# Optimization experiments

Hardware: AMD Instinct MI355X
Metric: run time of the kernel (lower is better)

Reference implementation:

```python
import jax, jax.numpy as jnp
import numpy as np

N, E, D_IN, HD, H = 50000, 800000, 768, 64, 4
HC = HD * H


def _gat(x, src, dst, etypes, lin_w, att_src, att_dst, edge_emb, lin_edge_w, att_edge,
         bias, res_w, res_b, ln_g, ln_b):
    # Faithful PyG GATConv (edge_dim, concat=True, add_self_loops=True with
    # fill_value='mean', negative_slope=0.2) + residual + LayerNorm. Eval mode: no dropout.
    n = x.shape[0]
    h, c = att_src.shape
    xs = (x @ lin_w).reshape(n, h, c)                      # [N,H,C]
    a_src = jnp.einsum('nhc,hc->nh', xs, att_src)          # [N,H]
    a_dst = jnp.einsum('nhc,hc->nh', xs, att_dst)
    eattr = edge_emb[etypes]                               # [E,ed]
    ones = jnp.ones((etypes.shape[0],), x.dtype)
    cnt = jax.ops.segment_sum(ones, dst, num_segments=n)
    # self-loop edge_attr = mean of incoming edge attrs per node (fill_value='mean')
    loop_attr = jax.ops.segment_sum(eattr, dst, num_segments=n) / jnp.maximum(cnt, 1.0)[:, None]
    loop = jnp.arange(n, dtype=src.dtype)
    src_a = jnp.concatenate([src, loop])
    dst_a = jnp.concatenate([dst, loop])
    e_all = jnp.concatenate([eattr, loop_attr], 0)
    a_edge = jnp.einsum('ehc,hc->eh', (e_all @ lin_edge_w).reshape(-1, h, c), att_edge)
    alpha = jax.nn.leaky_relu(a_src[src_a] + a_dst[dst_a] + a_edge, 0.2)   # [Ea,H]
    # edge softmax over incoming edges of each destination node
    amax = jax.ops.segment_max(alpha, dst_a, num_segments=n)
    ea = jnp.exp(alpha - amax[dst_a])
    denom = jax.ops.segment_sum(ea, dst_a, num_segments=n)
    w = ea / (denom[dst_a] + 1e-16)
    out = jax.ops.segment_sum(xs[src_a] * w[:, :, None], dst_a, num_segments=n)
    out = out.reshape(n, h * c) + bias + (x @ res_w + res_b)
    mu = out.mean(-1, keepdims=True)
    var = jnp.mean((out - mu) ** 2, -1, keepdims=True)
    return (out - mu) * jax.lax.rsqrt(var + 1e-5) * ln_g + ln_b


def _forward(features, positions,
             fe_w1, fe_b1, fe_w2, fe_b2, fe_pos_w, fe_pos_b, fe_type_emb, fe_out_w, fe_out_b,
             g1_lin_w, g1_att_src, g1_att_dst, g1_edge_emb, g1_lin_edge_w, g1_att_edge,
             g1_bias, g1_res_w, g1_res_b, g1_ln_g, g1_ln_b,
             g2_lin_w, g2_att_src, g2_att_dst, g2_edge_emb, g2_lin_edge_w, g2_att_edge,
             g2_bias, g2_res_w, g2_res_b, g2_ln_g, g2_ln_b,
             cls_w, cls_b,
             edge_index, aspect_indices, edge_types, node_types):
    # EnhancedFeatureExtractor (eval: dropout = identity)
    hfe = jax.nn.relu(features @ fe_w1 + fe_b1) @ fe_w2 + fe_b2
    hfe = hfe + fe_type_emb[node_types] + positions[:, None] @ fe_pos_w + fe_pos_b
    hfe = hfe @ fe_out_w + fe_out_b
    src, dst = edge_index[0], edge_index[1]
    hid = _gat(hfe, src, dst, edge_types, g1_lin_w, g1_att_src, g1_att_dst, g1_edge_emb,
               g1_lin_edge_w, g1_att_edge, g1_bias, g1_res_w, g1_res_b, g1_ln_g, g1_ln_b)
    hid = jax.nn.relu(hid)
    hid = _gat(hid, src, dst, edge_types, g2_lin_w, g2_att_src, g2_att_dst, g2_edge_emb,
               g2_lin_edge_w, g2_att_edge, g2_bias, g2_res_w, g2_res_b, g2_ln_g, g2_ln_b)
    return hid[aspect_indices] @ cls_w + cls_b


def setup_inputs() -> dict:
    key = jax.random.key(0)
    ks = jax.random.split(key, 40)
    d = {}
    d['features'] = jax.random.normal(ks[0], (N, D_IN), jnp.float32)
    d['edge_index'] = jax.random.randint(ks[1], (2, E), 0, N, jnp.int32)
    d['aspect_indices'] = jax.random.randint(ks[2], (4096,), 0, N, jnp.int32)
    d['edge_types'] = jax.random.randint(ks[3], (E,), 0, 4, jnp.int32)
    d['node_types'] = jax.random.randint(ks[4], (N,), 0, 3, jnp.int32)
    d['positions'] = jax.random.uniform(ks[5], (N,), jnp.float32)

    def rn(i, shape, s=0.05):
        return s * jax.random.normal(ks[i], shape, jnp.float32)

    d['fe_w1'] = rn(6, (D_IN, HD)); d['fe_b1'] = rn(7, (HD,))
    d['fe_w2'] = rn(8, (HD, HD));   d['fe_b2'] = rn(9, (HD,))
    d['fe_pos_w'] = rn(10, (1, HD)); d['fe_pos_b'] = rn(11, (HD,))
    d['fe_type_emb'] = rn(12, (3, HD))
    d['fe_out_w'] = rn(13, (HD, HD)); d['fe_out_b'] = rn(14, (HD,))
    d['g1_lin_w'] = rn(15, (HD, HC))
    d['g1_att_src'] = rn(16, (H, HD)); d['g1_att_dst'] = rn(17, (H, HD))
    d['g1_edge_emb'] = rn(18, (4, 4)); d['g1_lin_edge_w'] = rn(19, (4, HC))
    d['g1_att_edge'] = rn(20, (H, HD))
    d['g1_bias'] = rn(21, (HC,)); d['g1_res_w'] = rn(22, (HD, HC)); d['g1_res_b'] = rn(23, (HC,))
    d['g1_ln_g'] = jnp.ones((HC,), jnp.float32); d['g1_ln_b'] = jnp.zeros((HC,), jnp.float32)
    d['g2_lin_w'] = rn(24, (HC, HD))
    d['g2_att_src'] = rn(25, (1, HD)); d['g2_att_dst'] = rn(26, (1, HD))
    d['g2_edge_emb'] = rn(27, (4, 4)); d['g2_lin_edge_w'] = rn(28, (4, HD))
    d['g2_att_edge'] = rn(29, (1, HD))
    d['g2_bias'] = rn(30, (HD,)); d['g2_res_w'] = rn(31, (HC, HD)); d['g2_res_b'] = rn(32, (HD,))
    d['g2_ln_g'] = jnp.ones((HD,), jnp.float32); d['g2_ln_b'] = jnp.zeros((HD,), jnp.float32)
    d['cls_w'] = rn(33, (HD, 3)); d['cls_b'] = rn(34, (3,))
    return d


def reference(features, edge_index, aspect_indices, edge_types, node_types, positions,
              fe_w1, fe_b1, fe_w2, fe_b2, fe_pos_w, fe_pos_b, fe_type_emb, fe_out_w, fe_out_b,
              g1_lin_w, g1_att_src, g1_att_dst, g1_edge_emb, g1_lin_edge_w, g1_att_edge,
              g1_bias, g1_res_w, g1_res_b, g1_ln_g, g1_ln_b,
              g2_lin_w, g2_att_src, g2_att_dst, g2_edge_emb, g2_lin_edge_w, g2_att_edge,
              g2_bias, g2_res_w, g2_res_b, g2_ln_g, g2_ln_b,
              cls_w, cls_b):
    return _forward(features, positions,
                    fe_w1, fe_b1, fe_w2, fe_b2, fe_pos_w, fe_pos_b, fe_type_emb, fe_out_w, fe_out_b,
                    g1_lin_w, g1_att_src, g1_att_dst, g1_edge_emb, g1_lin_edge_w, g1_att_edge,
                    g1_bias, g1_res_w, g1_res_b, g1_ln_g, g1_ln_b,
                    g2_lin_w, g2_att_src, g2_att_dst, g2_edge_emb, g2_lin_edge_w, g2_att_edge,
                    g2_bias, g2_res_w, g2_res_b, g2_ln_g, g2_ln_b,
                    cls_w, cls_b,
                    edge_index, aspect_indices, edge_types, node_types)
```

## Files before the change

kernel.cpp:

```cpp
#include <hip/hip_runtime.h>


#define LRELU(x) ((x) > 0.f ? (x) : 0.2f * (x))

typedef __attribute__((ext_vector_type(8))) short short8;
typedef __attribute__((ext_vector_type(4))) float floatx4;

__device__ __forceinline__ unsigned short f2bf(float x) {
    union { float f; unsigned int u; } v; v.f = x;
    unsigned int r = (v.u + 0x7FFFu + ((v.u >> 16) & 1u)) >> 16;
    return (unsigned short)r;
}
__device__ __forceinline__ float bflo(unsigned int u) {
    return __uint_as_float(u << 16);
}
__device__ __forceinline__ float bfhi(unsigned int u) {
    return __uint_as_float(u & 0xFFFF0000u);
}
__device__ __forceinline__ float bf1(unsigned short u) {
    return __uint_as_float(((unsigned int)u) << 16);
}

__global__ __launch_bounds__(64) void k_tables(
    const float* __restrict__ e_emb1, const float* __restrict__ lew1,
    const float* __restrict__ ae1,
    const float* __restrict__ e_emb2, const float* __restrict__ lew2,
    const float* __restrict__ ae2,
    float* __restrict__ aet1, float* __restrict__ aet2)
{
    __shared__ float M1[16];
    __shared__ float M2[4];
    int t = threadIdx.x;
    if (t < 16) {
        int d = t >> 2, h = t & 3;
        float s = 0.f;
        for (int c = 0; c < 64; ++c) s += lew1[d * 256 + h * 64 + c] * ae1[h * 64 + c];
        M1[d * 4 + h] = s;
    }
    if (t < 4) {
        float s = 0.f;
        for (int c = 0; c < 64; ++c) s += lew2[t * 64 + c] * ae2[c];
        M2[t] = s;
    }
    __syncthreads();
    if (t < 16) {
        int ty = t >> 2, h = t & 3;
        float s = 0.f;
        for (int d = 0; d < 4; ++d) s += e_emb1[ty * 4 + d] * M1[d * 4 + h];
        aet1[ty * 4 + h] = s;
    }
    if (t < 4) {
        float s = 0.f;
        for (int d = 0; d < 4; ++d) s += e_emb2[t * 4 + d] * M2[d];
        aet2[t] = s;
    }
}

__global__ __launch_bounds__(256) void k_fe1(
    const float* __restrict__ feat, const float* __restrict__ w1,
    const float* __restrict__ b1, float* __restrict__ t1, int N)
{
    __shared__ __align__(16) unsigned short A_lds[8 * 64 * 8];
    __shared__ __align__(16) unsigned short B_lds[8 * 64 * 8];
    int t = threadIdx.x;
    int wv = t >> 6, lane = t & 63;
    int quad = lane >> 4, l16 = lane & 15;
    long n0 = (long)blockIdx.x * 64;

    floatx4 acc[4];
#pragma unroll
    for (int i = 0; i < 4; ++i) acc[i] = (floatx4){0.f, 0.f, 0.f, 0.f};

    int srow = t >> 2;
    int sf4 = t & 3;
    long arow = n0 + srow;
    if (arow >= N) arow = N - 1;
    const float* fbase = feat + arow * 768;

    for (int kc = 0; kc < 768; kc += 64) {
        __syncthreads();
#pragma unroll
        for (int i = 0; i < 4; ++i) {
            int f = sf4 + i * 4;
            int kl = f * 4;
            float4 v = *(const float4*)(fbase + kc + kl);
            int kg = kl >> 3, ko = kl & 7;
            unsigned short* d = &A_lds[(kg * 64 + srow) * 8 + ko];
            ushort4 pk = {f2bf(v.x), f2bf(v.y), f2bf(v.z), f2bf(v.w)};
            *(ushort4*)d = pk;
        }
#pragma unroll
        for (int i = 0; i < 4; ++i) {
            int f = sf4 + i * 4;
            int nl = f * 4;
            int kl = srow;
            float4 v = *(const float4*)(w1 + (long)(kc + kl) * 64 + nl);
            int kg = kl >> 3, j = kl & 7;
            B_lds[(kg * 64 + nl + 0) * 8 + j] = f2bf(v.x);
            B_lds[(kg * 64 + nl + 1) * 8 + j] = f2bf(v.y);
            B_lds[(kg * 64 + nl + 2) * 8 + j] = f2bf(v.z);
            B_lds[(kg * 64 + nl + 3) * 8 + j] = f2bf(v.w);
        }
        __syncthreads();
#pragma unroll
        for (int s = 0; s < 2; ++s) {
            int kg0 = s * 4 + quad;
            short8 bfrag = *(const short8*)&B_lds[(kg0 * 64 + wv * 16 + l16) * 8];
#pragma unroll
            for (int mt = 0; mt < 4; ++mt) {
                short8 afrag = *(const short8*)&A_lds[(kg0 * 64 + mt * 16 + l16) * 8];
                acc[mt] = __builtin_amdgcn_mfma_f32_16x16x32_bf16(
                    afrag, bfrag, acc[mt], 0, 0, 0);
            }
        }
    }
    int col = wv * 16 + l16;
    float bb = b1[col];
#pragma unroll
    for (int mt = 0; mt < 4; ++mt) {
#pragma unroll
        for (int r = 0; r < 4; ++r) {
            long m = n0 + mt * 16 + quad * 4 + r;
            if (m < N) t1[m * 64 + col] = fmaxf(acc[mt][r] + bb, 0.f);
        }
    }
}

__global__ __launch_bounds__(256) void k_fe2(
    const float* __restrict__ t1, const float* __restrict__ w2,
    const float* __restrict__ b2, const int* __restrict__ ntypes,
    const float* __restrict__ temb, const float* __restrict__ pos,
    const float* __restrict__ posw, const float* __restrict__ posb,
    const float* __restrict__ outw, const float* __restrict__ outb,
    float* __restrict__ hfe)
{
    __shared__ float l1[256];
    __shared__ float l2[256];
    int t = threadIdx.x;
    long base = (long)blockIdx.x * 256;
    l1[t] = t1[base + t];
    __syncthreads();
    int r = t >> 6, c = t & 63;
    float acc = 0.f;
#pragma unroll 8
    for (int k = 0; k < 64; ++k) acc += l1[r * 64 + k] * w2[k * 64 + c];
    long n = (long)blockIdx.x * 4 + r;
    int nt = ntypes[n];
    acc += b2[c] + temb[nt * 64 + c] + pos[n] * posw[c] + posb[c];
    l2[r * 64 + c] = acc;
    __syncthreads();
    float acc2 = 0.f;
#pragma unroll 8
    for (int k = 0; k < 64; ++k) acc2 += l2[r * 64 + k] * outw[k * 64 + c];
    hfe[n * 64 + c] = acc2 + outb[c];
}

template<int K, int NH>
__global__ __launch_bounds__(256) void k_prep_gemm(
    const float* __restrict__ A, const float* __restrict__ B1,
    const float* __restrict__ B2, const float* __restrict__ bias,
    const float* __restrict__ res_b, unsigned short* __restrict__ xsb,
    float* __restrict__ resp, int N)
{
    __shared__ __align__(16) unsigned short A_lds[8 * 64 * 8];
    __shared__ __align__(16) unsigned short B_lds[8 * 128 * 8];
    int t = threadIdx.x;
    int wv = t >> 6, lane = t & 63;
    int quad = lane >> 4, l16 = lane & 15;
    long n0 = (long)blockIdx.x * 64;
    int gcol0 = blockIdx.y * 128;

    floatx4 acc[4][2];
#pragma unroll
    for (int i = 0; i < 4; ++i)
#pragma unroll
        for (int j = 0; j < 2; ++j) acc[i][j] = (floatx4){0.f, 0.f, 0.f, 0.f};

    int srow = t >> 2, sf4 = t & 3;
    long arow = n0 + srow;
    if (arow >= N) arow = N - 1;
    const float* abase = A + arow * (long)K;
    int bk0 = t >> 5;
    int bc4 = t & 31;

    for (int kc = 0; kc < K; kc += 64) {
        __syncthreads();
#pragma unroll
        for (int i = 0; i < 4; ++i) {
            int f = sf4 + i * 4;
            int kl = f * 4;
            float4 v = *(const float4*)(abase + kc + kl);
            int kg = kl >> 3, ko = kl & 7;
            ushort4 pk = {f2bf(v.x), f2bf(v.y), f2bf(v.z), f2bf(v.w)};
            *(ushort4*)&A_lds[(kg * 64 + srow) * 8 + ko] = pk;
        }
#pragma unroll
        for (int i = 0; i < 8; ++i) {
            int kl = bk0 + i * 8;
            int col4 = bc4 * 4;
            int gc = gcol0 + col4;
            const float* bsrc = (gc < NH) ? (B1 + (long)(kc + kl) * NH + gc)
                                          : (B2 + (long)(kc + kl) * NH + gc - NH);
            float4 v = *(const float4*)bsrc;
            int kg = kl >> 3, j = kl & 7;
            B_lds[(kg * 128 + col4 + 0) * 8 + j] = f2bf(v.x);
            B_lds[(kg * 128 + col4 + 1) * 8 + j] = f2bf(v.y);
            B_lds[(kg * 128 + col4 + 2) * 8 + j] = f2bf(v.z);
            B_lds[(kg * 128 + col4 + 3) * 8 + j] = f2bf(v.w);
        }
        __syncthreads();
#pragma unroll
        for (int s = 0; s < 2; ++s) {
            int kg0 = s * 4 + quad;
#pragma unroll
            for (int nt = 0; nt < 2; ++nt) {
                short8 bfrag = *(const short8*)&B_lds[(kg0 * 128 + wv * 32 + nt * 16 + l16) * 8];
#pragma unroll
                for (int mt = 0; mt < 4; ++mt) {
                    short8 afrag = *(const short8*)&A_lds[(kg0 * 64 + mt * 16 + l16) * 8];
                    acc[mt][nt] = __builtin_amdgcn_mfma_f32_16x16x32_bf16(
                        afrag, bfrag, acc[mt][nt], 0, 0, 0);
                }
            }
        }
    }
#pragma unroll
    for (int nt = 0; nt < 2; ++nt) {
        int gc = gcol0 + wv * 32 + nt * 16 + l16;
        bool isl = gc < NH;
        int oc = isl ? gc : gc - NH;
        float badd = isl ? 0.f : (bias[oc] + res_b[oc]);
#pragma unroll
        for (int mt = 0; mt < 4; ++mt) {
#pragma unroll
            for (int r = 0; r < 4; ++r) {
                long m = n0 + mt * 16 + quad * 4 + r;
                if (m < N) {
                    float val = acc[mt][nt][r];
                    if (isl) xsb[m * NH + oc] = f2bf(val);
                    else     resp[m * NH + oc] = val + badd;
                }
            }
        }
    }
}

template<int H>
__global__ __launch_bounds__(256) void k_att(
    const unsigned short* __restrict__ xsb, const float* __restrict__ att_s,
    const float* __restrict__ att_d, float* __restrict__ a_src,
    float* __restrict__ a_dst, int N)
{
    int t = threadIdx.x;
    int wv = t >> 6, lane = t & 63;
    long n = (long)blockIdx.x * 4 + wv;
    if (n >= N) return;
    if (H == 4) {
        ushort4 u = *(const ushort4*)&xsb[n * 256 + lane * 4];
        float4 as = *(const float4*)&att_s[lane * 4];
        float4 ad = *(const float4*)&att_d[lane * 4];
        float x0 = bf1(u.x), x1 = bf1(u.y), x2 = bf1(u.z), x3 = bf1(u.w);
        float p = x0 * as.x + x1 * as.y + x2 * as.z + x3 * as.w;
        float q = x0 * ad.x + x1 * ad.y + x2 * ad.z + x3 * ad.w;
#pragma unroll
        for (int k = 8; k; k >>= 1) {
            p += __shfl_xor(p, k, 64);
            q += __shfl_xor(q, k, 64);
        }
        if ((lane & 15) == 0) {
            a_src[n * 4 + (lane >> 4)] = p;
            a_dst[n * 4 + (lane >> 4)] = q;
        }
    } else {
        float x = bf1(xsb[n * 64 + lane]);
        float p = x * att_s[lane];
        float q = x * att_d[lane];
#pragma unroll
        for (int k = 32; k; k >>= 1) {
            p += __shfl_xor(p, k, 64);
            q += __shfl_xor(q, k, 64);
        }
        if (lane == 0) { a_src[n] = p; a_dst[n] = q; }
    }
}

__global__ __launch_bounds__(256) void k_count(
    const int* __restrict__ dst, const int* __restrict__ et,
    int* __restrict__ cnt_t, int E)
{
    int e = blockIdx.x * 256 + threadIdx.x;
    if (e < E) atomicAdd(&cnt_t[dst[e] * 4 + et[e]], 1);
}

__global__ __launch_bounds__(256) void k_scan1(
    const int* __restrict__ cnt_t, int* __restrict__ row_off,
    int* __restrict__ blk_sums, int N)
{
    __shared__ int s[256];
    int t = threadIdx.x;
    int i = blockIdx.x * 256 + t;
    int v = 0;
    if (i < N) v = cnt_t[4 * i] + cnt_t[4 * i + 1] + cnt_t[4 * i + 2] + cnt_t[4 * i + 3];
    s[t] = v;
    __syncthreads();
    for (int off = 1; off < 256; off <<= 1) {
        int x = 0;
        if (t >= off) x = s[t - off];
        __syncthreads();
        s[t] += x;
        __syncthreads();
    }
    if (i < N) row_off[i] = s[t] - v;
    if (t == 255) blk_sums[blockIdx.x] = s[255];
}

__global__ __launch_bounds__(256) void k_scan2(int* __restrict__ blk_sums, int nb)
{
    __shared__ int s[256];
    int t = threadIdx.x;
    int v = (t < nb) ? blk_sums[t] : 0;
    s[t] = v;
    __syncthreads();
    for (int off = 1; off < 256; off <<= 1) {
        int x = 0;
        if (t >= off) x = s[t - off];
        __syncthreads();
        s[t] += x;
        __syncthreads();
    }
    if (t < nb) blk_sums[t] = s[t] - v;
}

__global__ __launch_bounds__(256) void k_scan3(
    int* __restrict__ row_off, int* __restrict__ cursor,
    const int* __restrict__ blk_sums, int N, int E)
{
    int t = threadIdx.x;
    int i = blockIdx.x * 256 + t;
    if (i < N) {
        int o = row_off[i] + blk_sums[blockIdx.x];
        row_off[i] = o;
        cursor[i] = o;
    }
    if (i == 0) row_off[N] = E;
}

__global__ __launch_bounds__(256) void k_scatter(
    const int* __restrict__ src, const int* __restrict__ dst,
    const int* __restrict__ et, int* __restrict__ cursor,
    int* __restrict__ csr_pack, int E)
{
    int e = blockIdx.x * 256 + threadIdx.x;
    if (e < E) {
        int d = dst[e];
        int pos = atomicAdd(&cursor[d], 1);
        csr_pack[pos] = src[e] | (et[e] << 28);
    }
}

__global__ __launch_bounds__(128) void k_gat1(
    const unsigned short* __restrict__ xs1b, const float* __restrict__ a_src,
    const float* __restrict__ a_dst, const int* __restrict__ row_off,
    const int* __restrict__ csr_pack,
    const int* __restrict__ cnt_t, const float* __restrict__ aet1,
    const float* __restrict__ ln_g, const float* __restrict__ ln_b,
    float* io)
{
    __shared__ __align__(16) float4 ws[2][64];
    __shared__ float2 aetp[2][4];
    __shared__ float red[4];
    int n = blockIdx.x;
    int t = threadIdx.x;
    int w = t >> 6, c = t & 63;
    int h0 = 2 * w;
    if (t < 8) {
        int w2 = t >> 2, ty = t & 3;
        aetp[w2][ty] = make_float2(aet1[ty * 4 + 2 * w2], aet1[ty * 4 + 2 * w2 + 1]);
    }
    int off = row_off[n], deg = row_off[n + 1] - off;
    float2 a_d = *(const float2*)&a_dst[n * 4 + h0];
    __syncthreads();
    float ael0 = 0.f, ael1 = 0.f;
    int degc = 0;
#pragma unroll
    for (int ty = 0; ty < 4; ++ty) {
        int ct = cnt_t[n * 4 + ty];
        degc += ct;
        float2 ae = aetp[w][ty];
        ael0 += (float)ct * ae.x;
        ael1 += (float)ct * ae.y;
    }
    float inv = (degc > 0) ? 1.f / (float)degc : 1.f;
    float2 a_s_self = *(const float2*)&a_src[n * 4 + h0];
    float al0 = a_s_self.x + a_d.x + ael0 * inv;
    float al1 = a_s_self.y + a_d.y + ael1 * inv;
    al0 = LRELU(al0); al1 = LRELU(al1);
    float wself0 = expf(al0), wself1 = expf(al1);
    int col = w * 128 + 2 * c;
    unsigned int uself = *(const unsigned int*)&xs1b[(long)n * 256 + col];
    float wself_l = (c < 32) ? wself0 : wself1;
    float acc0 = wself_l * bflo(uself);
    float acc1 = wself_l * bfhi(uself);
    float dp0 = 0.f, dp1 = 0.f;
    const unsigned short* xcol = xs1b + col;
    for (int base = 0; base < deg; base += 64) {
        int cnt = min(64, deg - base);
        if (c < cnt) {
            int pk = csr_pack[off + base + c];
            int s = pk & 0x0FFFFFFF;
            int ty = ((unsigned)pk) >> 28;
            float2 as2 = *(const float2*)&a_src[s * 4 + h0];
            float2 ae = aetp[w][ty];
            float a0 = as2.x + a_d.x + ae.x;
            float a1 = as2.y + a_d.y + ae.y;
            a0 = LRELU(a0); a1 = LRELU(a1);
            float w0 = expf(a0), w1 = expf(a1);
            dp0 += w0; dp1 += w1;
            ws[w][c] = make_float4(w0, w1, __int_as_float(s), 0.f);
        }
        int i = 0;
        float b00 = 0.f, b01 = 0.f, b10 = 0.f, b11 = 0.f;
        for (; i + 2 <= cnt; i += 2) {
            float4 p0 = ws[w][i];
            float4 p1 = ws[w][i + 1];
            unsigned int u0 = *(const unsigned int*)&xcol[(long)__float_as_int(p0.z) * 256];
            unsigned int u1 = *(const unsigned int*)&xcol[(long)__float_as_int(p1.z) * 256];
            float w0 = (c < 32) ? p0.x : p0.y;
            float w1 = (c < 32) ? p1.x : p1.y;
            b00 += w0 * bflo(u0); b01 += w0 * bfhi(u0);
            b10 += w1 * bflo(u1); b11 += w1 * bfhi(u1);
        }
        if (i < cnt) {
            float4 p = ws[w][i];
            unsigned int u = *(const unsigned int*)&xcol[(long)__float_as_int(p.z) * 256];
            float w0 = (c < 32) ? p.x : p.y;
            b00 += w0 * bflo(u); b01 += w0 * bfhi(u);
        }
        acc0 += b00 + b10;
        acc1 += b01 + b11;
    }
#pragma unroll
    for (int k = 32; k; k >>= 1) {
        dp0 += __shfl_xor(dp0, k, 64);
        dp1 += __shfl_xor(dp1, k, 64);
    }
    float dsum = ((c < 32) ? dp0 + wself0 : dp1 + wself1) + 1e-16f;
    float2 res = *(const float2*)&io[(long)n * 256 + col];
    float v0 = acc0 / dsum + res.x;
    float v1 = acc1 / dsum + res.y;
    float s1 = v0 + v1, s2 = v0 * v0 + v1 * v1;
#pragma unroll
    for (int k = 32; k; k >>= 1) {
        s1 += __shfl_xor(s1, k, 64);
        s2 += __shfl_xor(s2, k, 64);
    }
    if (c == 0) { red[w] = s1; red[2 + w] = s2; }
    __syncthreads();
    float mu = (red[0] + red[1]) * (1.f / 256.f);
    float var = (red[2] + red[3]) * (1.f / 256.f) - mu * mu;
    float rs = rsqrtf(var + 1e-5f);
    float2 g = *(const float2*)&ln_g[col];
    float2 bln = *(const float2*)&ln_b[col];
    float y0 = fmaxf((v0 - mu) * rs * g.x + bln.x, 0.f);
    float y1 = fmaxf((v1 - mu) * rs * g.y + bln.y, 0.f);
    *(float2*)&io[(long)n * 256 + col] = make_float2(y0, y1);
}

__global__ __launch_bounds__(64) void k_gat2(
    const unsigned short* __restrict__ xs2b, const float* __restrict__ a_src,
    const float* __restrict__ a_dst, const int* __restrict__ row_off,
    const int* __restrict__ csr_pack,
    const int* __restrict__ cnt_t, const float* __restrict__ aet2,
    const float* __restrict__ ln_g, const float* __restrict__ ln_b,
    float* io)
{
    __shared__ __align__(8) float2 ws[64];
    __shared__ float aetl[4];
    int n = blockIdx.x;
    int c = threadIdx.x;
    if (c < 4) aetl[c] = aet2[c];
    int off = row_off[n], deg = row_off[n + 1] - off;
    float a_d = a_dst[n];
    float ael = 0.f;
    int degc = 0;
#pragma unroll
    for (int ty = 0; ty < 4; ++ty) {
        int ct = cnt_t[n * 4 + ty];
        degc += ct;
        ael += (float)ct * aet2[ty];
    }
    ael *= (degc > 0 ? 1.f / (float)degc : 1.f);
    float al = a_src[n] + a_d + ael;
    al = LRELU(al);
    float wself = expf(al);
    float acc = wself * bf1(xs2b[(long)n * 64 + c]);
    float dp = 0.f;
    const unsigned short* xcol = xs2b + c;
    for (int base = 0; base < deg; base += 64) {
        int cnt = min(64, deg - base);
        if (c < cnt) {
            int pk = csr_pack[off + base + c];
            int s = pk & 0x0FFFFFFF;
            int ty = ((unsigned)pk) >> 28;
            float a = a_src[s] + a_d + aetl[ty];
            a = LRELU(a);
            float we = expf(a);
            dp += we;
            ws[c] = make_float2(we, __int_as_float(s));
        }
        int i = 0;
        float b0 = 0.f, b1 = 0.f;
        for (; i + 2 <= cnt; i += 2) {
            float2 p0 = ws[i];
            float2 p1 = ws[i + 1];
            b0 += p0.x * bf1(xcol[(long)__float_as_int(p0.y) * 64]);
            b1 += p1.x * bf1(xcol[(long)__float_as_int(p1.y) * 64]);
        }
        if (i < cnt) {
            float2 p = ws[i];
            b0 += p.x * bf1(xcol[(long)__float_as_int(p.y) * 64]);
        }
        acc += b0 + b1;
    }
#pragma unroll
    for (int k = 32; k; k >>= 1) dp += __shfl_xor(dp, k, 64);
    float dsum = dp + wself + 1e-16f;
    float v = acc / dsum + io[(long)n * 64 + c];
    float s1 = v, s2 = v * v;
#pragma unroll
    for (int k = 32; k; k >>= 1) {
        s1 += __shfl_xor(s1, k, 64);
        s2 += __shfl_xor(s2, k, 64);
    }
    float mu = s1 * (1.f / 64.f);
    float var = s2 * (1.f / 64.f) - mu * mu;
    io[(long)n * 64 + c] = (v - mu) * rsqrtf(var + 1e-5f) * ln_g[c] + ln_b[c];
}

__global__ __launch_bounds__(256) void k_cls(
    const float* __restrict__ hid2, const int* __restrict__ asp,
    const float* __restrict__ w, const float* __restrict__ b,
    float* __restrict__ out)
{
    int g = blockIdx.x * 256 + threadIdx.x;
    int i = g / 3, j = g - i * 3;
    int a = asp[i];
    float acc = b[j];
#pragma unroll 8
    for (int cc = 0; cc < 64; ++cc) acc += hid2[(long)a * 64 + cc] * w[cc * 3 + j];
    out[i * 3 + j] = acc;
}

extern "C" void kernel_launch(void* const* d_in, const int* in_sizes, int n_in,
                              void* d_out, int out_size, void* d_ws, size_t ws_size,
                              hipStream_t stream)
{
    const float* features    = (const float*)d_in[0];
    const int*   edge_index  = (const int*)d_in[1];
    const int*   aspect      = (const int*)d_in[2];
    const int*   etypes      = (const int*)d_in[3];
    const int*   ntypes      = (const int*)d_in[4];
    const float* pos         = (const float*)d_in[5];
    const float* fe_w1       = (const float*)d_in[6];
    const float* fe_b1       = (const float*)d_in[7];
    const float* fe_w2       = (const float*)d_in[8];
    const float* fe_b2       = (const float*)d_in[9];
    const float* fe_pos_w    = (const float*)d_in[10];
    const float* fe_pos_b    = (const float*)d_in[11];
    const float* fe_type_emb = (const float*)d_in[12];
    const float* fe_out_w    = (const float*)d_in[13];
    const float* fe_out_b    = (const float*)d_in[14];
    const float* g1_lin_w    = (const float*)d_in[15];
    const float* g1_att_src  = (const float*)d_in[16];
    const float* g1_att_dst  = (const float*)d_in[17];
    const float* g1_edge_emb = (const float*)d_in[18];
    const float* g1_lin_edge = (const float*)d_in[19];
    const float* g1_att_edge = (const float*)d_in[20];
    const float* g1_bias     = (const float*)d_in[21];
    const float* g1_res_w    = (const float*)d_in[22];
    const float* g1_res_b    = (const float*)d_in[23];
    const float* g1_ln_g     = (const float*)d_in[24];
    const float* g1_ln_b     = (const float*)d_in[25];
    const float* g2_lin_w    = (const float*)d_in[26];
    const float* g2_att_src  = (const float*)d_in[27];
    const float* g2_att_dst  = (const float*)d_in[28];
    const float* g2_edge_emb = (const float*)d_in[29];
    const float* g2_lin_edge = (const float*)d_in[30];
    const float* g2_att_edge = (const float*)d_in[31];
    const float* g2_bias     = (const float*)d_in[32];
    const float* g2_res_w    = (const float*)d_in[33];
    const float* g2_res_b    = (const float*)d_in[34];
    const float* g2_ln_g     = (const float*)d_in[35];
    const float* g2_ln_b     = (const float*)d_in[36];
    const float* cls_w       = (const float*)d_in[37];
    const float* cls_b       = (const float*)d_in[38];

    const int N = in_sizes[0] / 768;
    const int E = in_sizes[1] / 2;
    const int* src = edge_index;
    const int* dst = edge_index + E;

    char* wsb = (char*)d_ws;
    size_t off = 0;
    auto alloc = [&](size_t bytes) -> char* {
        char* p = wsb + off;
        off += (bytes + 255) & ~(size_t)255;
        return p;
    };
    float* t1      = (float*)alloc((size_t)N * 64 * 4);
    float* hfe     = (float*)alloc((size_t)N * 64 * 4);
    unsigned short* xs1b = (unsigned short*)alloc((size_t)N * 256 * 2);
    unsigned short* xs2b = (unsigned short*)alloc((size_t)N * 64 * 2);
    float* rp1     = (float*)alloc((size_t)N * 256 * 4);
    float* rp2     = (float*)alloc((size_t)N * 64 * 4);
    float* a_src1  = (float*)alloc((size_t)N * 4 * 4);
    float* a_dst1  = (float*)alloc((size_t)N * 4 * 4);
    float* a_src2  = (float*)alloc((size_t)N * 4);
    float* a_dst2  = (float*)alloc((size_t)N * 4);
    int*   cnt_t   = (int*)alloc((size_t)N * 4 * 4);
    int*   row_off = (int*)alloc((size_t)(N + 1) * 4);
    int*   cursor  = (int*)alloc((size_t)N * 4);
    int*   blk     = (int*)alloc(1024);
    int*   csr_pack= (int*)alloc((size_t)E * 4);
    float* aet1    = (float*)alloc(64);
    float* aet2    = (float*)alloc(64);

    hipMemsetAsync(cnt_t, 0, (size_t)N * 4 * 4, stream);

    int mb = (N + 63) / 64;
    int ab = (N + 3) / 4;

    k_tables<<<1, 64, 0, stream>>>(g1_edge_emb, g1_lin_edge, g1_att_edge,
                                   g2_edge_emb, g2_lin_edge, g2_att_edge, aet1, aet2);
    k_fe1<<<mb, 256, 0, stream>>>(features, fe_w1, fe_b1, t1, N);
    k_fe2<<<N / 4, 256, 0, stream>>>(t1, fe_w2, fe_b2, ntypes, fe_type_emb, pos,
                                     fe_pos_w, fe_pos_b, fe_out_w, fe_out_b, hfe);
    k_prep_gemm<64, 256><<<dim3(mb, 4), 256, 0, stream>>>(
        hfe, g1_lin_w, g1_res_w, g1_bias, g1_res_b, xs1b, rp1, N);
    k_att<4><<<ab, 256, 0, stream>>>(xs1b, g1_att_src, g1_att_dst, a_src1, a_dst1, N);
    int eblk = (E + 255) / 256;
    int nb = (N + 255) / 256;
    k_count<<<eblk, 256, 0, stream>>>(dst, etypes, cnt_t, E);
    k_scan1<<<nb, 256, 0, stream>>>(cnt_t, row_off, blk, N);
    k_scan2<<<1, 256, 0, stream>>>(blk, nb);
    k_scan3<<<nb, 256, 0, stream>>>(row_off, cursor, blk, N, E);
    k_scatter<<<eblk, 256, 0, stream>>>(src, dst, etypes, cursor, csr_pack, E);
    k_gat1<<<N, 128, 0, stream>>>(xs1b, a_src1, a_dst1, row_off, csr_pack,
                                  cnt_t, aet1, g1_ln_g, g1_ln_b, rp1);
    k_prep_gemm<256, 64><<<dim3(mb, 1), 256, 0, stream>>>(
        rp1, g2_lin_w, g2_res_w, g2_bias, g2_res_b, xs2b, rp2, N);
    k_att<1><<<ab, 256, 0, stream>>>(xs2b, g2_att_src, g2_att_dst, a_src2, a_dst2, N);
    k_gat2<<<N, 64, 0, stream>>>(xs2b, a_src2, a_dst2, row_off, csr_pack,
                                 cnt_t, aet2, g2_ln_g, g2_ln_b, rp2);
    k_cls<<<(out_size + 255) / 256, 256, 0, stream>>>(rp2, aspect, cls_w, cls_b,
                                                      (float*)d_out);
}
```

Measured before the change: 699.3 us.

## Pre-swizzle GEMM weights to bf16 fragments and unroll padded GAT aggregation

Adds small kernels that convert the weight matrices once per call into a bf16 MFMA-fragment layout. The GEMMs then read B fragments straight from global memory instead of restaging and converting them through LDS in every block. A-tile conversion now uses packed bf16 stores via perm, which rounds half-up instead of to nearest-even. The GAT aggregation loops pad to multiples of 8 with zero-weight entries and fully unroll, trading a few wasted gathers for more memory-level parallelism.

```diff
diff --git a/kernel.cpp b/kernel.cpp
--- a/kernel.cpp
+++ b/kernel.cpp
@@ -10,6 +10,11 @@
     union { float f; unsigned int u; } v; v.f = x;
     unsigned int r = (v.u + 0x7FFFu + ((v.u >> 16) & 1u)) >> 16;
     return (unsigned short)r;
+}
+__device__ __forceinline__ unsigned int pkbf(float lo, float hi) {
+    unsigned int a = __float_as_uint(lo) + 0x8000u;
+    unsigned int b = __float_as_uint(hi) + 0x8000u;
+    return __builtin_amdgcn_perm(b, a, 0x07060302u);
 }
 __device__ __forceinline__ float bflo(unsigned int u) {
     return __uint_as_float(u << 16);
@@ -56,12 +61,38 @@
     }
 }
 
+__global__ __launch_bounds__(256) void k_bswz_fe1(
+    const float* __restrict__ w1, unsigned short* __restrict__ out)
+{
+    for (int idx = blockIdx.x * 256 + threadIdx.x; idx < 768 * 64;
+         idx += gridDim.x * 256) {
+        int k = idx >> 6, col = idx & 63;
+        int c = k >> 6, kl = k & 63, kg = kl >> 3, j = kl & 7;
+        out[((c * 8 + kg) * 64 + col) * 8 + j] = f2bf(w1[k * 64 + col]);
+    }
+}
+
+template<int K, int NH>
+__global__ __launch_bounds__(256) void k_bswz2(
+    const float* __restrict__ B1, const float* __restrict__ B2,
+    unsigned short* __restrict__ out)
+{
+    const int NC = 2 * NH;
+    for (int idx = blockIdx.x * 256 + threadIdx.x; idx < K * NC;
+         idx += gridDim.x * 256) {
+        int k = idx / NC, col = idx % NC;
+        float v = (col < NH) ? B1[k * NH + col] : B2[k * NH + col - NH];
+        int c = k >> 6, kl = k & 63, kg = kl >> 3, j = kl & 7;
+        int ct = col >> 7, cl = col & 127;
+        out[(((c * (NC / 128) + ct) * 8 + kg) * 128 + cl) * 8 + j] = f2bf(v);
+    }
+}
+
 __global__ __launch_bounds__(256) void k_fe1(
-    const float* __restrict__ feat, const float* __restrict__ w1,
+    const float* __restrict__ feat, const unsigned short* __restrict__ bswz,
     const float* __restrict__ b1, float* __restrict__ t1, int N)
 {
     __shared__ __align__(16) unsigned short A_lds[8 * 64 * 8];
-    __shared__ __align__(16) unsigned short B_lds[8 * 64 * 8];
     int t = threadIdx.x;
     int wv = t >> 6, lane = t & 63;
     int quad = lane >> 4, l16 = lane & 15;
@@ -71,41 +102,30 @@
 #pragma unroll
     for (int i = 0; i < 4; ++i) acc[i] = (floatx4){0.f, 0.f, 0.f, 0.f};
 
-    int srow = t >> 2;
-    int sf4 = t & 3;
+    int srow = t >> 2, sf4 = t & 3;
     long arow = n0 + srow;
     if (arow >= N) arow = N - 1;
-    const float* fbase = feat + arow * 768;
+    const float* fbase = feat + arow * 768 + sf4 * 16;
+    int col = wv * 16 + l16;
 
     for (int kc = 0; kc < 768; kc += 64) {
         __syncthreads();
-#pragma unroll
-        for (int i = 0; i < 4; ++i) {
-            int f = sf4 + i * 4;
-            int kl = f * 4;
-            float4 v = *(const float4*)(fbase + kc + kl);
-            int kg = kl >> 3, ko = kl & 7;
-            unsigned short* d = &A_lds[(kg * 64 + srow) * 8 + ko];
-            ushort4 pk = {f2bf(v.x), f2bf(v.y), f2bf(v.z), f2bf(v.w)};
-            *(ushort4*)d = pk;
-        }
-#pragma unroll
-        for (int i = 0; i < 4; ++i) {
-            int f = sf4 + i * 4;
-            int nl = f * 4;
-            int kl = srow;
-            float4 v = *(const float4*)(w1 + (long)(kc + kl) * 64 + nl);
-            int kg = kl >> 3, j = kl & 7;
-            B_lds[(kg * 64 + nl + 0) * 8 + j] = f2bf(v.x);
-            B_lds[(kg * 64 + nl + 1) * 8 + j] = f2bf(v.y);
-            B_lds[(kg * 64 + nl + 2) * 8 + j] = f2bf(v.z);
-            B_lds[(kg * 64 + nl + 3) * 8 + j] = f2bf(v.w);
-        }
-        __syncthreads();
+        float4 v0 = *(const float4*)(fbase + kc);
+        float4 v1 = *(const float4*)(fbase + kc + 4);
+        float4 v2 = *(const float4*)(fbase + kc + 8);
+        float4 v3 = *(const float4*)(fbase + kc + 12);
+        uint4 w0 = {pkbf(v0.x, v0.y), pkbf(v0.z, v0.w),
+                    pkbf(v1.x, v1.y), pkbf(v1.z, v1.w)};
+        uint4 w1p = {pkbf(v2.x, v2.y), pkbf(v2.z, v2.w),
+                     pkbf(v3.x, v3.y), pkbf(v3.z, v3.w)};
+        *(uint4*)&A_lds[((2 * sf4) * 64 + srow) * 8] = w0;
+        *(uint4*)&A_lds[((2 * sf4 + 1) * 64 + srow) * 8] = w1p;
+        __syncthreads();
+        int ci = kc >> 6;
 #pragma unroll
         for (int s = 0; s < 2; ++s) {
             int kg0 = s * 4 + quad;
-            short8 bfrag = *(const short8*)&B_lds[(kg0 * 64 + wv * 16 + l16) * 8];
+            short8 bfrag = *(const short8*)&bswz[((ci * 8 + kg0) * 64 + col) * 8];
 #pragma unroll
             for (int mt = 0; mt < 4; ++mt) {
                 short8 afrag = *(const short8*)&A_lds[(kg0 * 64 + mt * 16 + l16) * 8];
@@ -114,7 +134,6 @@
             }
         }
     }
-    int col = wv * 16 + l16;
     float bb = b1[col];
 #pragma unroll
     for (int mt = 0; mt < 4; ++mt) {
@@ -157,18 +176,17 @@
 
 template<int K, int NH>
 __global__ __launch_bounds__(256) void k_prep_gemm(
-    const float* __restrict__ A, const float* __restrict__ B1,
-    const float* __restrict__ B2, const float* __restrict__ bias,
-    const float* __restrict__ res_b, unsigned short* __restrict__ xsb,
-    float* __restrict__ resp, int N)
-{
+    const float* __restrict__ A, const unsigned short* __restrict__ bswz,
+    const float* __restrict__ bias, const float* __restrict__ res_b,
+    unsigned short* __restrict__ xsb, float* __restrict__ resp, int N)
+{
+    constexpr int CT = (2 * NH) / 128;
     __shared__ __align__(16) unsigned short A_lds[8 * 64 * 8];
-    __shared__ __align__(16) unsigned short B_lds[8 * 128 * 8];
     int t = threadIdx.x;
     int wv = t >> 6, lane = t & 63;
     int quad = lane >> 4, l16 = lane & 15;
     long n0 = (long)blockIdx.x * 64;
-    int gcol0 = blockIdx.y * 128;
+    int by = blockIdx.y;
 
     floatx4 acc[4][2];
 #pragma unroll
@@ -179,42 +197,29 @@
     int srow = t >> 2, sf4 = t & 3;
     long arow = n0 + srow;
     if (arow >= N) arow = N - 1;
-    const float* abase = A + arow * (long)K;
-    int bk0 = t >> 5;
-    int bc4 = t & 31;
+    const float* abase = A + arow * (long)K + sf4 * 16;
 
     for (int kc = 0; kc < K; kc += 64) {
         __syncthreads();
-#pragma unroll
-        for (int i = 0; i < 4; ++i) {
-            int f = sf4 + i * 4;
-            int kl = f * 4;
-            float4 v = *(const float4*)(abase + kc + kl);
-            int kg = kl >> 3, ko = kl & 7;
-            ushort4 pk = {f2bf(v.x), f2bf(v.y), f2bf(v.z), f2bf(v.w)};
-            *(ushort4*)&A_lds[(kg * 64 + srow) * 8 + ko] = pk;
-        }
-#pragma unroll
-        for (int i = 0; i < 8; ++i) {
-            int kl = bk0 + i * 8;
-            int col4 = bc4 * 4;
-            int gc = gcol0 + col4;
-            const float* bsrc = (gc < NH) ? (B1 + (long)(kc + kl) * NH + gc)
-                                          : (B2 + (long)(kc + kl) * NH + gc - NH);
-            float4 v = *(const float4*)bsrc;
-            int kg = kl >> 3, j = kl & 7;
-            B_lds[(kg * 128 + col4 + 0) * 8 + j] = f2bf(v.x);
-            B_lds[(kg * 128 + col4 + 1) * 8 + j] = f2bf(v.y);
-            B_lds[(kg * 128 + col4 + 2) * 8 + j] = f2bf(v.z);
-            B_lds[(kg * 128 + col4 + 3) * 8 + j] = f2bf(v.w);
-        }
-        __syncthreads();
+        float4 v0 = *(const float4*)(abase + kc);
+        float4 v1 = *(const float4*)(abase + kc + 4);
+        float4 v2 = *(const float4*)(abase + kc + 8);
+        float4 v3 = *(const float4*)(abase + kc + 12);
+        uint4 w0 = {pkbf(v0.x, v0.y), pkbf(v0.z, v0.w),
+                    pkbf(v1.x, v1.y), pkbf(v1.z, v1.w)};
+        uint4 w1p = {pkbf(v2.x, v2.y), pkbf(v2.z, v2.w),
+                     pkbf(v3.x, v3.y), pkbf(v3.z, v3.w)};
+        *(uint4*)&A_lds[((2 * sf4) * 64 + srow) * 8] = w0;
+        *(uint4*)&A_lds[((2 * sf4 + 1) * 64 + srow) * 8] = w1p;
+        __syncthreads();
+        int ci = kc >> 6;
 #pragma unroll
         for (int s = 0; s < 2; ++s) {
             int kg0 = s * 4 + quad;
 #pragma unroll
             for (int nt = 0; nt < 2; ++nt) {
-                short8 bfrag = *(const short8*)&B_lds[(kg0 * 128 + wv * 32 + nt * 16 + l16) * 8];
+                short8 bfrag = *(const short8*)&bswz[
+                    (((ci * CT + by) * 8 + kg0) * 128 + wv * 32 + nt * 16 + l16) * 8];
 #pragma unroll
                 for (int mt = 0; mt < 4; ++mt) {
                     short8 afrag = *(const short8*)&A_lds[(kg0 * 64 + mt * 16 + l16) * 8];
@@ -226,7 +231,7 @@
     }
 #pragma unroll
     for (int nt = 0; nt < 2; ++nt) {
-        int gc = gcol0 + wv * 32 + nt * 16 + l16;
+        int gc = by * 128 + wv * 32 + nt * 16 + l16;
         bool isl = gc < NH;
         int oc = isl ? gc : gc - NH;
         float badd = isl ? 0.f : (bias[oc] + res_b[oc]);
@@ -405,39 +410,33 @@
     const unsigned short* xcol = xs1b + col;
     for (int base = 0; base < deg; base += 64) {
         int cnt = min(64, deg - base);
+        float w0 = 0.f, w1 = 0.f;
+        int s = 0;
         if (c < cnt) {
             int pk = csr_pack[off + base + c];
-            int s = pk & 0x0FFFFFFF;
+            s = pk & 0x0FFFFFFF;
             int ty = ((unsigned)pk) >> 28;
             float2 as2 = *(const float2*)&a_src[s * 4 + h0];
             float2 ae = aetp[w][ty];
             float a0 = as2.x + a_d.x + ae.x;
             float a1 = as2.y + a_d.y + ae.y;
             a0 = LRELU(a0); a1 = LRELU(a1);
-            float w0 = expf(a0), w1 = expf(a1);
-            dp0 += w0; dp1 += w1;
-            ws[w][c] = make_float4(w0, w1, __int_as_float(s), 0.f);
-        }
-        int i = 0;
-        float b00 = 0.f, b01 = 0.f, b10 = 0.f, b11 = 0.f;
-        for (; i + 2 <= cnt; i += 2) {
-            float4 p0 = ws[w][i];
-            float4 p1 = ws[w][i + 1];
-            unsigned int u0 = *(const unsigned int*)&xcol[(long)__float_as_int(p0.z) * 256];
-            unsigned int u1 = *(const unsigned int*)&xcol[(long)__float_as_int(p1.z) * 256];
-            float w0 = (c < 32) ? p0.x : p0.y;
-            float w1 = (c < 32) ? p1.x : p1.y;
-            b00 += w0 * bflo(u0); b01 += w0 * bfhi(u0);
-            b10 += w1 * bflo(u1); b11 += w1 * bfhi(u1);
-        }
-        if (i < cnt) {
-            float4 p = ws[w][i];
-            unsigned int u = *(const unsigned int*)&xcol[(long)__float_as_int(p.z) * 256];
-            float w0 = (c < 32) ? p.x : p.y;
-            b00 += w0 * bflo(u); b01 += w0 * bfhi(u);
-        }
-        acc0 += b00 + b10;
-        acc1 += b01 + b11;
+            w0 = expf(a0); w1 = expf(a1);
+        }
+        dp0 += w0; dp1 += w1;
+        ws[w][c] = make_float4(w0, w1, __int_as_float(s), 0.f);
+        int cr = (cnt + 7) & ~7;
+        for (int i = 0; i < cr; i += 8) {
+#pragma unroll
+            for (int u = 0; u < 8; ++u) {
+                float4 p = ws[w][i + u];
+                unsigned int uu = *(const unsigned int*)&xcol[
+                    (long)__float_as_int(p.z) * 256];
+                float wl = (c < 32) ? p.x : p.y;
+                acc0 += wl * bflo(uu);
+                acc1 += wl * bfhi(uu);
+            }
+        }
     }
 #pragma unroll
     for (int k = 32; k; k >>= 1) {
@@ -498,29 +497,26 @@
     const unsigned short* xcol = xs2b + c;
     for (int base = 0; base < deg; base += 64) {
         int cnt = min(64, deg - base);
+        float we = 0.f;
+        int s = 0;
         if (c < cnt) {
             int pk = csr_pack[off + base + c];
-            int s = pk & 0x0FFFFFFF;
+            s = pk & 0x0FFFFFFF;
             int ty = ((unsigned)pk) >> 28;
             float a = a_src[s] + a_d + aetl[ty];
             a = LRELU(a);
-            float we = expf(a);
-            dp += we;
-            ws[c] = make_float2(we, __int_as_float(s));
-        }
-        int i = 0;
-        float b0 = 0.f, b1 = 0.f;
-        for (; i + 2 <= cnt; i += 2) {
-            float2 p0 = ws[i];
-            float2 p1 = ws[i + 1];
-            b0 += p0.x * bf1(xcol[(long)__float_as_int(p0.y) * 64]);
-            b1 += p1.x * bf1(xcol[(long)__float_as_int(p1.y) * 64]);
-        }
-        if (i < cnt) {
-            float2 p = ws[i];
-            b0 += p.x * bf1(xcol[(long)__float_as_int(p.y) * 64]);
-        }
-        acc += b0 + b1;
+            we = expf(a);
+        }
+        dp += we;
+        ws[c] = make_float2(we, __int_as_float(s));
+        int cr = (cnt + 7) & ~7;
+        for (int i = 0; i < cr; i += 8) {
+#pragma unroll
+            for (int u = 0; u < 8; ++u) {
+                float2 p = ws[i + u];
+                acc += p.x * bf1(xcol[(long)__float_as_int(p.y) * 64]);
+            }
+        }
     }
 #pragma unroll
     for (int k = 32; k; k >>= 1) dp += __shfl_xor(dp, k, 64);
@@ -624,6 +620,9 @@
     int*   csr_pack= (int*)alloc((size_t)E * 4);
     float* aet1    = (float*)alloc(64);
     float* aet2    = (float*)alloc(64);
+    unsigned short* bz_fe1 = (unsigned short*)alloc(768 * 64 * 2);
+    unsigned short* bz_p1  = (unsigned short*)alloc(64 * 512 * 2);
+    unsigned short* bz_p2  = (unsigned short*)alloc(256 * 128 * 2);
 
     hipMemsetAsync(cnt_t, 0, (size_t)N * 4 * 4, stream);
 
@@ -632,11 +631,14 @@
 
     k_tables<<<1, 64, 0, stream>>>(g1_edge_emb, g1_lin_edge, g1_att_edge,
                                    g2_edge_emb, g2_lin_edge, g2_att_edge, aet1, aet2);
-    k_fe1<<<mb, 256, 0, stream>>>(features, fe_w1, fe_b1, t1, N);
+    k_bswz_fe1<<<48, 256, 0, stream>>>(fe_w1, bz_fe1);
+    k_bswz2<64, 256><<<32, 256, 0, stream>>>(g1_lin_w, g1_res_w, bz_p1);
+    k_bswz2<256, 64><<<32, 256, 0, stream>>>(g2_lin_w, g2_res_w, bz_p2);
+    k_fe1<<<mb, 256, 0, stream>>>(features, bz_fe1, fe_b1, t1, N);
     k_fe2<<<N / 4, 256, 0, stream>>>(t1, fe_w2, fe_b2, ntypes, fe_type_emb, pos,
                                      fe_pos_w, fe_pos_b, fe_out_w, fe_out_b, hfe);
     k_prep_gemm<64, 256><<<dim3(mb, 4), 256, 0, stream>>>(
-        hfe, g1_lin_w, g1_res_w, g1_bias, g1_res_b, xs1b, rp1, N);
+        hfe, bz_p1, g1_bias, g1_res_b, xs1b, rp1, N);
     k_att<4><<<ab, 256, 0, stream>>>(xs1b, g1_att_src, g1_att_dst, a_src1, a_dst1, N);
     int eblk = (E + 255) / 256;
     int nb = (N + 255) / 256;
@@ -648,7 +650,7 @@
     k_gat1<<<N, 128, 0, stream>>>(xs1b, a_src1, a_dst1, row_off, csr_pack,
                                   cnt_t, aet1, g1_ln_g, g1_ln_b, rp1);
     k_prep_gemm<256, 64><<<dim3(mb, 1), 256, 0, stream>>>(
-        rp1, g2_lin_w, g2_res_w, g2_bias, g2_res_b, xs2b, rp2, N);
+        rp1, bz_p2, g2_bias, g2_res_b, xs2b, rp2, N);
     k_att<1><<<ab, 256, 0, stream>>>(xs2b, g2_att_src, g2_att_dst, a_src2, a_dst2, N);
     k_gat2<<<N, 64, 0, stream>>>(xs2b, a_src2, a_dst2, row_off, csr_pack,
                                  cnt_t, aet2, g2_ln_g, g2_ln_b, rp2);
```

New measurement: 638.7 us. 1.09x faster.
